# Kernel optimization log

Measured on AMD Instinct MI355X. Metric: run time of the kernel, lower is better.

The kernel has to match this reference:

```python
import jax, jax.numpy as jnp
import numpy as np

DIM = 768      # model dim
H = 12         # heads
HD = DIM // H  # head dim = 64
T = 8          # num_frames // 2 (video temporal frames)
SF = 8         # spec_frames (audio temporal frames)
AP = 196       # audio patches per frame
VP = 196       # video patches per frame
B = 4          # batch
SCALE = HD ** (-0.5)  # 0.125


def setup_inputs() -> dict:
    key = jax.random.key(0)
    ks = jax.random.split(key, 12)
    n = lambda k, shape, s=1.0: s * jax.random.normal(k, shape, dtype=jnp.float32)
    return {
        "s_x": n(ks[0], (2 + AP, B * SF, DIM)),
        "t_x": n(ks[1], (1 + VP, B * T, DIM)),
        "clip_space_pos": n(ks[2], (AP, DIM), SCALE),
        "vmae_space_pos": n(ks[3], (VP, DIM), SCALE),
        "clip_temporal_pos": n(ks[4], (SF, DIM), SCALE),
        "vmae_temporal_pos": n(ks[5], (T, DIM), SCALE),
        "q_w": n(ks[6], (DIM, DIM), 0.02),
        "q_b": jnp.zeros((DIM,), jnp.float32),
        "kv_w": n(ks[7], (2 * DIM, DIM), 0.02),
        "kv_b": jnp.zeros((2 * DIM,), jnp.float32),
        "proj_w": n(ks[8], (DIM, DIM), 0.02),
        "proj_b": jnp.zeros((DIM,), jnp.float32),
    }


def _prep(pat, space_pos, temp_pos, tt):
    # pat: (n, b*tt, d) ; rearrange 'n (b t) d -> b t n d', add space pos,
    # 'b t n d -> b n t d', add temporal pos, 'b n t d -> b (n t) d'
    n, bt, d = pat.shape
    b = bt // tt
    x = pat.reshape(n, b, tt, d).transpose(1, 2, 0, 3)      # b t n d
    x = x + space_pos                                        # (n,d) bcast
    x = x.transpose(0, 2, 1, 3) + temp_pos                   # b n t d + (t,d)
    return x.reshape(b, n * tt, d)


def reference(s_x, t_x, clip_space_pos, vmae_space_pos, clip_temporal_pos,
              vmae_temporal_pos, q_w, q_b, kv_w, kv_b, proj_w, proj_b):
    t_x_cls = t_x[:1]                                        # (1, b*T, d)
    s_pat = _prep(s_x[2:], clip_space_pos, clip_temporal_pos, SF)   # (b, AP*SF, d)
    t_pat = _prep(t_x[1:], vmae_space_pos, vmae_temporal_pos, T)    # (b, VP*T, d)

    b, N, d = t_pat.shape
    M = s_pat.shape[1]
    q = t_pat @ q_w.T + q_b                                  # (b, N, d)
    q = q.reshape(b, N, H, HD).transpose(0, 2, 1, 3)         # b h n hd
    kv = s_pat @ kv_w.T + kv_b                               # (b, M, 2d)
    kv = kv.reshape(b, M, 2, H, HD).transpose(2, 0, 3, 1, 4) # 2 b h m hd
    k, v = kv[0], kv[1]

    attn = jax.nn.softmax(jnp.einsum('bhnd,bhmd->bhnm', q * SCALE, k), axis=-1)
    out = jnp.einsum('bhnm,bhmd->bhnd', attn, v)             # b h n hd
    out = out.transpose(0, 2, 1, 3).reshape(b, N, d)         # b n d
    out = out @ proj_w.T + proj_b

    # 'b (n t) d -> n (b t) d'
    out = out.reshape(b, VP, T, d).transpose(1, 0, 2, 3).reshape(VP, b * T, d)
    return jnp.concatenate([t_x_cls, out], axis=0)           # (1+VP, b*T, d)
```

## Files before the change

kernel.cpp:

```cpp
#include <hip/hip_runtime.h>
#include <hip/hip_bf16.h>

#define DIM 768
#define NH 12
#define HD 64
#define NSEQ 1568
#define ROWS 6272
#define QSC2 0.18033688011112042f
#define AST 72

typedef __attribute__((ext_vector_type(8))) short short8;
typedef __attribute__((ext_vector_type(4))) float f32x4;
typedef __attribute__((ext_vector_type(4))) unsigned short u16x4;
typedef unsigned short ushort_t;
typedef unsigned int uint_t;

static __device__ __forceinline__ ushort_t f2bf(float f) {
    union { float f; uint_t u; } c; c.f = f;
    uint_t u = c.u + 0x7fffu + ((c.u >> 16) & 1u);
    return (ushort_t)(u >> 16);
}
static __device__ __forceinline__ int cvt_pk_bf16(float lo, float hi) {
    int r;
    asm("v_cvt_pk_bf16_f32 %0, %1, %2" : "=v"(r) : "v"(lo), "v"(hi));
    return r;
}
static __device__ __forceinline__ void glds16(const short* g, short* l) {
    __builtin_amdgcn_global_load_lds(
        (const __attribute__((address_space(1))) void*)g,
        (__attribute__((address_space(3))) void*)l, 16, 0, 0);
}

#define PREP_HALF (ROWS * (DIM / 8))
__global__ __launch_bounds__(256)
void prep2_bf(const float* __restrict__ src_t, const float* __restrict__ src_s,
              const float* __restrict__ vsp, const float* __restrict__ csp,
              const float* __restrict__ vtp, const float* __restrict__ ctp,
              short* __restrict__ dst_t, short* __restrict__ dst_s) {
    int idx = blockIdx.x * 256 + threadIdx.x;
    if (idx >= 2 * PREP_HALF) return;
    int sel = idx >= PREP_HALF;
    int i0  = sel ? idx - PREP_HALF : idx;
    const float* src  = sel ? src_s : src_t;
    const float* spos = sel ? csp : vsp;
    const float* tpos = sel ? ctp : vtp;
    short* dst = sel ? dst_s : dst_t;
    int d8  = i0 % (DIM / 8);
    int row = i0 / (DIM / 8);
    int b = row / NSEQ;
    int i = row % NSEQ;
    int n = i >> 3;
    int t = i & 7;
    const float4* s4 = reinterpret_cast<const float4*>(src + ((size_t)n * 32 + b * 8 + t) * DIM + d8 * 8);
    const float4* p4 = reinterpret_cast<const float4*>(spos + (size_t)n * DIM + d8 * 8);
    const float4* q4 = reinterpret_cast<const float4*>(tpos + (size_t)t * DIM + d8 * 8);
    union { int w[4]; short8 v; } o;
    float4 a0 = s4[0], a1 = s4[1], b0 = p4[0], b1 = p4[1], c0 = q4[0], c1 = q4[1];
    o.w[0] = cvt_pk_bf16(a0.x + b0.x + c0.x, a0.y + b0.y + c0.y);
    o.w[1] = cvt_pk_bf16(a0.z + b0.z + c0.z, a0.w + b0.w + c0.w);
    o.w[2] = cvt_pk_bf16(a1.x + b1.x + c1.x, a1.y + b1.y + c1.y);
    o.w[3] = cvt_pk_bf16(a1.z + b1.z + c1.z, a1.w + b1.w + c1.w);
    reinterpret_cast<short8*>(dst)[i0] = o.v;
}

#define W8 (DIM * DIM / 8)
__global__ __launch_bounds__(256)
void conv3_bf(const float* __restrict__ qw, const float* __restrict__ kvw,
              const float* __restrict__ pw, short* __restrict__ dq,
              short* __restrict__ dkv, short* __restrict__ dp) {
    int idx = blockIdx.x * 256 + threadIdx.x;
    if (idx >= 4 * W8) return;
    const float* src; short* dst; int off;
    if (idx < W8)            { src = qw;  dst = dq;  off = idx; }
    else if (idx < 3 * W8)   { src = kvw; dst = dkv; off = idx - W8; }
    else                     { src = pw;  dst = dp;  off = idx - 3 * W8; }
    const float4* s4 = reinterpret_cast<const float4*>(src + (size_t)off * 8);
    float4 a0 = s4[0], a1 = s4[1];
    union { int w[4]; short8 v; } o;
    o.w[0] = cvt_pk_bf16(a0.x, a0.y);
    o.w[1] = cvt_pk_bf16(a0.z, a0.w);
    o.w[2] = cvt_pk_bf16(a1.x, a1.y);
    o.w[3] = cvt_pk_bf16(a1.z, a1.w);
    reinterpret_cast<short8*>(dst)[off] = o.v;
}

__global__ __launch_bounds__(256)
void cls_kernel(const float* __restrict__ src, float* __restrict__ dst) {
    int idx = blockIdx.x * 256 + threadIdx.x;
    if (idx < 32 * DIM / 4)
        reinterpret_cast<float4*>(idx + (float4*)dst)[0] = reinterpret_cast<const float4*>(src)[idx];
}

__global__ __launch_bounds__(256)
void gemm_qkv(const short* __restrict__ tpat, const short* __restrict__ spat,
              const short* __restrict__ wq, const short* __restrict__ wkv,
              const float* __restrict__ q_b, const float* __restrict__ kv_b,
              ushort_t* __restrict__ qout, ushort_t* __restrict__ kout,
              ushort_t* __restrict__ vtout) {
    __shared__ short As[128 * 32];
    __shared__ short Ws[128 * 32];
    const int t = threadIdx.x;
    const int l = t & 63, w = t >> 6;
    const int li = l & 15, g = l >> 4;
    const int mode = (blockIdx.x >= 6);
    const short* A  = mode ? spat : tpat;
    const short* Wm = mode ? wkv : wq;
    const float* bias = mode ? kv_b : q_b;
    const int c0 = (mode ? (int)blockIdx.x - 6 : (int)blockIdx.x) * 128;
    const int r0 = blockIdx.y * 128;
    const int wrow = (w >> 1) * 64, wcol = (w & 1) * 64;

    f32x4 acc[4][4];
    #pragma unroll
    for (int i = 0; i < 4; ++i)
        #pragma unroll
        for (int j = 0; j < 4; ++j) acc[i][j] = (f32x4){0.f, 0.f, 0.f, 0.f};

    const short* Ag = A  + (size_t)(r0 + w * 32 + (l >> 2)) * DIM + (l & 3) * 8;
    const short* Wg = Wm + (size_t)(c0 + w * 32 + (l >> 2)) * DIM + (l & 3) * 8;
    short* Al0 = &As[(w * 32) * 32];
    short* Al1 = &As[(w * 32 + 16) * 32];
    short* Wl0 = &Ws[(w * 32) * 32];
    short* Wl1 = &Ws[(w * 32 + 16) * 32];

    for (int k0 = 0; k0 < DIM; k0 += 32) {
        glds16(Ag + k0,                       Al0);
        glds16(Ag + (size_t)16 * DIM + k0,    Al1);
        glds16(Wg + k0,                       Wl0);
        glds16(Wg + (size_t)16 * DIM + k0,    Wl1);
        __syncthreads();
        short8 af[4], wf[4];
        #pragma unroll
        for (int mi = 0; mi < 4; ++mi)
            af[mi] = *reinterpret_cast<const short8*>(&As[(wrow + mi * 16 + li) * 32 + g * 8]);
        #pragma unroll
        for (int ni = 0; ni < 4; ++ni)
            wf[ni] = *reinterpret_cast<const short8*>(&Ws[(wcol + ni * 16 + li) * 32 + g * 8]);
        __builtin_amdgcn_s_setprio(1);
        #pragma unroll
        for (int mi = 0; mi < 4; ++mi)
            #pragma unroll
            for (int ni = 0; ni < 4; ++ni)
                acc[mi][ni] = __builtin_amdgcn_mfma_f32_16x16x32_bf16(af[mi], wf[ni], acc[mi][ni], 0, 0, 0);
        __builtin_amdgcn_s_setprio(0);
        __syncthreads();
    }

    #pragma unroll
    for (int mi = 0; mi < 4; ++mi) {
        int rowbase = r0 + wrow + mi * 16 + g * 4;
        int b = rowbase / NSEQ;
        int ii = rowbase - b * NSEQ;
        #pragma unroll
        for (int ni = 0; ni < 4; ++ni) {
            int c = c0 + wcol + ni * 16 + li;
            float bv = bias[c];
            if (mode == 0) {
                int h = c >> 6, e = c & 63;
                size_t base = (((size_t)b * NH + h) * NSEQ + ii) * HD + e;
                #pragma unroll
                for (int rr = 0; rr < 4; ++rr)
                    qout[base + (size_t)rr * HD] = f2bf((acc[mi][ni][rr] + bv) * QSC2);
            } else {
                if (c < DIM) {
                    int h = c >> 6, e = c & 63;
                    size_t base = (((size_t)b * NH + h) * NSEQ + ii) * HD + e;
                    #pragma unroll
                    for (int rr = 0; rr < 4; ++rr)
                        kout[base + (size_t)rr * HD] = f2bf(acc[mi][ni][rr] + bv);
                } else {
                    int cc = c - DIM;
                    int h = cc >> 6, e = cc & 63;
                    union { int w2[2]; u16x4 v; } pk;
                    pk.w2[0] = cvt_pk_bf16(acc[mi][ni][0] + bv, acc[mi][ni][1] + bv);
                    pk.w2[1] = cvt_pk_bf16(acc[mi][ni][2] + bv, acc[mi][ni][3] + bv);
                    *reinterpret_cast<u16x4*>(vtout + (((size_t)b * NH + h) * HD + e) * NSEQ + ii) = pk.v;
                }
            }
        }
    }
}

__global__ __launch_bounds__(256)
void gemm_proj(const short* __restrict__ A, const short* __restrict__ Wm,
               const float* __restrict__ bias, float* __restrict__ out) {
    __shared__ short As[128 * 32];
    __shared__ short Ws[128 * 32];
    const int t = threadIdx.x;
    const int l = t & 63, w = t >> 6;
    const int li = l & 15, g = l >> 4;
    const int c0 = blockIdx.x * 128, r0 = blockIdx.y * 128;
    const int wrow = (w >> 1) * 64, wcol = (w & 1) * 64;

    f32x4 acc[4][4];
    #pragma unroll
    for (int i = 0; i < 4; ++i)
        #pragma unroll
        for (int j = 0; j < 4; ++j) acc[i][j] = (f32x4){0.f, 0.f, 0.f, 0.f};

    const short* Ag = A  + (size_t)(r0 + w * 32 + (l >> 2)) * DIM + (l & 3) * 8;
    const short* Wg = Wm + (size_t)(c0 + w * 32 + (l >> 2)) * DIM + (l & 3) * 8;
    short* Al0 = &As[(w * 32) * 32];
    short* Al1 = &As[(w * 32 + 16) * 32];
    short* Wl0 = &Ws[(w * 32) * 32];
    short* Wl1 = &Ws[(w * 32 + 16) * 32];

    for (int k0 = 0; k0 < DIM; k0 += 32) {
        glds16(Ag + k0,                       Al0);
        glds16(Ag + (size_t)16 * DIM + k0,    Al1);
        glds16(Wg + k0,                       Wl0);
        glds16(Wg + (size_t)16 * DIM + k0,    Wl1);
        __syncthreads();
        short8 af[4], wf[4];
        #pragma unroll
        for (int mi = 0; mi < 4; ++mi)
            af[mi] = *reinterpret_cast<const short8*>(&As[(wrow + mi * 16 + li) * 32 + g * 8]);
        #pragma unroll
        for (int ni = 0; ni < 4; ++ni)
            wf[ni] = *reinterpret_cast<const short8*>(&Ws[(wcol + ni * 16 + li) * 32 + g * 8]);
        __builtin_amdgcn_s_setprio(1);
        #pragma unroll
        for (int mi = 0; mi < 4; ++mi)
            #pragma unroll
            for (int ni = 0; ni < 4; ++ni)
                acc[mi][ni] = __builtin_amdgcn_mfma_f32_16x16x32_bf16(af[mi], wf[ni], acc[mi][ni], 0, 0, 0);
        __builtin_amdgcn_s_setprio(0);
        __syncthreads();
    }

    #pragma unroll
    for (int mi = 0; mi < 4; ++mi) {
        int rowbase = r0 + wrow + mi * 16 + g * 4;
        int b = rowbase / NSEQ;
        int ii = rowbase - b * NSEQ;
        #pragma unroll
        for (int ni = 0; ni < 4; ++ni) {
            int c = c0 + wcol + ni * 16 + li;
            float bv = bias[c];
            #pragma unroll
            for (int rr = 0; rr < 4; ++rr) {
                int i2 = ii + rr;
                int n = i2 >> 3, tt = i2 & 7;
                out[((size_t)(1 + n) * 32 + b * 8 + tt) * DIM + c] = acc[mi][ni][rr] + bv;
            }
        }
    }
}

__global__ __launch_bounds__(256)
void attn_bf(const short* __restrict__ q, const short* __restrict__ k,
             const short* __restrict__ vt, ushort_t* __restrict__ ao) {
    __shared__ short Qs[64 * AST];
    __shared__ short Ks[64 * AST];
    __shared__ short Vs[64 * AST];
    const int t = threadIdx.x, l = t & 63, w = t >> 6;
    const int li = l & 15, g = l >> 4;
    const int bh = blockIdx.y, b = bh / NH, h = bh % NH;
    const int q0 = blockIdx.x * 64;
    const short* qb = q + (size_t)bh * NSEQ * HD;
    const short* kb = k + (size_t)bh * NSEQ * HD;
    const short* vb = vt + (size_t)bh * HD * NSEQ;
    const int row = t >> 2, ch = t & 3;

    {
        int rs = (q0 + row < NSEQ) ? q0 + row : 0;
        const short* s = qb + (size_t)rs * HD + ch * 16;
        *reinterpret_cast<short8*>(&Qs[row * AST + ch * 16])     = *reinterpret_cast<const short8*>(s);
        *reinterpret_cast<short8*>(&Qs[row * AST + ch * 16 + 8]) = *reinterpret_cast<const short8*>(s + 8);
    }
    short8 kr0, kr1, vr0, vr1;
    {
        const short* s = kb + (size_t)row * HD + ch * 16;
        kr0 = *reinterpret_cast<const short8*>(s);
        kr1 = *reinterpret_cast<const short8*>(s + 8);
        const short* vs = vb + (size_t)row * NSEQ + ch * 16;
        vr0 = *reinterpret_cast<const short8*>(vs);
        vr1 = *reinterpret_cast<const short8*>(vs + 8);
    }
    __syncthreads();
    short8 qf[2];
    qf[0] = *reinterpret_cast<const short8*>(&Qs[(w * 16 + li) * AST + g * 8]);
    qf[1] = *reinterpret_cast<const short8*>(&Qs[(w * 16 + li) * AST + 32 + g * 8]);

    f32x4 oacc[4];
    #pragma unroll
    for (int i = 0; i < 4; ++i) oacc[i] = (f32x4){0.f, 0.f, 0.f, 0.f};
    float l_run = 0.f;
    const int addr0 = (li + ((2 * g) & 3) * 16) * 4;
    const int addr1 = (li + ((2 * g + 1) & 3) * 16) * 4;
    const int gh = g >> 1;

    for (int m0 = 0; m0 < NSEQ; m0 += 64) {
        *reinterpret_cast<short8*>(&Ks[row * AST + ch * 16])     = kr0;
        *reinterpret_cast<short8*>(&Ks[row * AST + ch * 16 + 8]) = kr1;
        *reinterpret_cast<short8*>(&Vs[row * AST + ch * 16])     = vr0;
        *reinterpret_cast<short8*>(&Vs[row * AST + ch * 16 + 8]) = vr1;
        __syncthreads();
        int m1 = m0 + 64;
        if (m1 < NSEQ) {
            int rs = (m1 + row < NSEQ) ? m1 + row : 0;
            const short* s = kb + (size_t)rs * HD + ch * 16;
            kr0 = *reinterpret_cast<const short8*>(s);
            kr1 = *reinterpret_cast<const short8*>(s + 8);
            int cs = (m1 + ch * 16 < NSEQ) ? ch : 0;
            const short* vs = vb + (size_t)row * NSEQ + m1 + cs * 16;
            vr0 = *reinterpret_cast<const short8*>(vs);
            vr1 = *reinterpret_cast<const short8*>(vs + 8);
        }

        f32x4 sacc[4];
        #pragma unroll
        for (int i = 0; i < 4; ++i) sacc[i] = (f32x4){0.f, 0.f, 0.f, 0.f};
        __builtin_amdgcn_s_setprio(1);
        #pragma unroll
        for (int jb = 0; jb < 4; ++jb) {
            short8 kf0 = *reinterpret_cast<const short8*>(&Ks[(jb * 16 + li) * AST + g * 8]);
            short8 kf1 = *reinterpret_cast<const short8*>(&Ks[(jb * 16 + li) * AST + 32 + g * 8]);
            sacc[jb] = __builtin_amdgcn_mfma_f32_16x16x32_bf16(kf0, qf[0], sacc[jb], 0, 0, 0);
            sacc[jb] = __builtin_amdgcn_mfma_f32_16x16x32_bf16(kf1, qf[1], sacc[jb], 0, 0, 0);
        }
        __builtin_amdgcn_s_setprio(0);
        if (m0 + 64 > NSEQ) {
            #pragma unroll
            for (int jb = 0; jb < 4; ++jb)
                #pragma unroll
                for (int r = 0; r < 4; ++r)
                    if (m0 + jb * 16 + g * 4 + r >= NSEQ) sacc[jb][r] = -1e30f;
        }

        float p[4][4];
        float ps[4];
        #pragma unroll
        for (int jb = 0; jb < 4; ++jb) {
            #pragma unroll
            for (int r = 0; r < 4; ++r)
                p[jb][r] = __builtin_amdgcn_exp2f(sacc[jb][r]);
            ps[jb] = (p[jb][0] + p[jb][1]) + (p[jb][2] + p[jb][3]);
        }
        float rowsum = (ps[0] + ps[1]) + (ps[2] + ps[3]);
        rowsum += __shfl_xor(rowsum, 16);
        rowsum += __shfl_xor(rowsum, 32);
        l_run += rowsum;

        int pw[4][2];
        #pragma unroll
        for (int jb = 0; jb < 4; ++jb) {
            pw[jb][0] = cvt_pk_bf16(p[jb][0], p[jb][1]);
            pw[jb][1] = cvt_pk_bf16(p[jb][2], p[jb][3]);
        }
        short8 pfrag[2];
        #pragma unroll
        for (int jb2 = 0; jb2 < 2; ++jb2) {
            int S0 = gh ? pw[jb2 * 2 + 1][0] : pw[jb2 * 2][0];
            int S1 = gh ? pw[jb2 * 2 + 1][1] : pw[jb2 * 2][1];
            union { int i[4]; short8 s; } fr;
            fr.i[0] = __builtin_amdgcn_ds_bpermute(addr0, S0);
            fr.i[1] = __builtin_amdgcn_ds_bpermute(addr0, S1);
            fr.i[2] = __builtin_amdgcn_ds_bpermute(addr1, S0);
            fr.i[3] = __builtin_amdgcn_ds_bpermute(addr1, S1);
            pfrag[jb2] = fr.s;
        }

        __builtin_amdgcn_s_setprio(1);
        #pragma unroll
        for (int nb = 0; nb < 4; ++nb)
            #pragma unroll
            for (int jb2 = 0; jb2 < 2; ++jb2) {
                short8 vf = *reinterpret_cast<const short8*>(&Vs[(nb * 16 + li) * AST + jb2 * 32 + g * 8]);
                oacc[nb] = __builtin_amdgcn_mfma_f32_16x16x32_bf16(vf, pfrag[jb2], oacc[nb], 0, 0, 0);
            }
        __builtin_amdgcn_s_setprio(0);
        __syncthreads();
    }

    int orow = q0 + w * 16 + li;
    if (orow < NSEQ) {
        float invl = 1.f / l_run;
        ushort_t* ob = ao + ((size_t)b * NSEQ + orow) * DIM + h * HD;
        #pragma unroll
        for (int nb = 0; nb < 4; ++nb) {
            union { int w2[2]; u16x4 v; } pk;
            pk.w2[0] = cvt_pk_bf16(oacc[nb][0] * invl, oacc[nb][1] * invl);
            pk.w2[1] = cvt_pk_bf16(oacc[nb][2] * invl, oacc[nb][3] * invl);
            *reinterpret_cast<u16x4*>(ob + nb * 16 + g * 4) = pk.v;
        }
    }
}

extern "C" void kernel_launch(void* const* d_in, const int* in_sizes, int n_in,
                              void* d_out, int out_size, void* d_ws, size_t ws_size,
                              hipStream_t stream) {
    const float* s_x    = (const float*)d_in[0];
    const float* t_x    = (const float*)d_in[1];
    const float* csp    = (const float*)d_in[2];
    const float* vsp    = (const float*)d_in[3];
    const float* ctp    = (const float*)d_in[4];
    const float* vtp    = (const float*)d_in[5];
    const float* q_w    = (const float*)d_in[6];
    const float* q_b    = (const float*)d_in[7];
    const float* kv_w   = (const float*)d_in[8];
    const float* kv_b   = (const float*)d_in[9];
    const float* proj_w = (const float*)d_in[10];
    const float* proj_b = (const float*)d_in[11];
    float* out = (float*)d_out;

    const size_t S2 = (size_t)ROWS * DIM;
    short* tpat = (short*)d_ws;
    short* spat = tpat + S2;
    short* qbf  = spat + S2;
    short* kbf  = qbf + S2;
    short* vtbf = kbf + S2;
    short* wq   = vtbf + S2;
    short* wkv  = wq + (size_t)DIM * DIM;
    short* wp   = wkv + (size_t)2 * DIM * DIM;

    prep2_bf<<<(2 * PREP_HALF + 255) / 256, 256, 0, stream>>>(
        t_x + (size_t)32 * DIM, s_x + (size_t)64 * DIM, vsp, csp, vtp, ctp, tpat, spat);
    conv3_bf<<<(4 * W8 + 255) / 256, 256, 0, stream>>>(q_w, kv_w, proj_w, wq, wkv, wp);
    cls_kernel<<<24, 256, 0, stream>>>(t_x, out);

    gemm_qkv<<<dim3(18, 49), 256, 0, stream>>>(tpat, spat, wq, wkv, q_b, kv_b,
                                               (ushort_t*)qbf, (ushort_t*)kbf, (ushort_t*)vtbf);
    attn_bf<<<dim3(25, 48), 256, 0, stream>>>(qbf, kbf, vtbf, (ushort_t*)tpat);
    gemm_proj<<<dim3(6, 49), 256, 0, stream>>>(tpat, wp, proj_b, out);
}
```

Baseline: 151.5 us.

## Double-buffer K/V in attention and process 32 query rows per warp

The attention kernel now handles 128 query rows per block (32 per warp as two 16-row halves), so each K/V tile staged in shared memory is reused across twice as many queries. K/V shared buffers are double-buffered, which leaves a single barrier per iteration and moves the next tile's LDS store ahead of the PV MFMAs. Q fragments are loaded straight from global memory into registers instead of passing through shared memory. The grid shrinks from 25 to 13 blocks in x, which halves the block count and raises per-thread register pressure, so occupancy may drop.

```diff
diff --git a/kernel.cpp b/kernel.cpp
--- a/kernel.cpp
+++ b/kernel.cpp
@@ -30,6 +30,41 @@
         (const __attribute__((address_space(1))) void*)g,
         (__attribute__((address_space(3))) void*)l, 16, 0, 0);
 }
+
+#define SM_HALF(S, PF, LR)                                                    \
+    {                                                                         \
+        float p_[4][4];                                                       \
+        _Pragma("unroll")                                                     \
+        for (int jb = 0; jb < 4; ++jb) {                                      \
+            _Pragma("unroll")                                                 \
+            for (int r = 0; r < 4; ++r)                                       \
+                p_[jb][r] = __builtin_amdgcn_exp2f(S[jb][r]);                 \
+        }                                                                     \
+        float rs_ = ((p_[0][0] + p_[0][1]) + (p_[0][2] + p_[0][3]))           \
+                  + ((p_[1][0] + p_[1][1]) + (p_[1][2] + p_[1][3]))           \
+                  + ((p_[2][0] + p_[2][1]) + (p_[2][2] + p_[2][3]))           \
+                  + ((p_[3][0] + p_[3][1]) + (p_[3][2] + p_[3][3]));          \
+        rs_ += __shfl_xor(rs_, 16);                                           \
+        rs_ += __shfl_xor(rs_, 32);                                           \
+        LR += rs_;                                                            \
+        int pw_[4][2];                                                        \
+        _Pragma("unroll")                                                     \
+        for (int jb = 0; jb < 4; ++jb) {                                      \
+            pw_[jb][0] = cvt_pk_bf16(p_[jb][0], p_[jb][1]);                   \
+            pw_[jb][1] = cvt_pk_bf16(p_[jb][2], p_[jb][3]);                   \
+        }                                                                     \
+        _Pragma("unroll")                                                     \
+        for (int jb2 = 0; jb2 < 2; ++jb2) {                                   \
+            int S0_ = gh ? pw_[jb2 * 2 + 1][0] : pw_[jb2 * 2][0];             \
+            int S1_ = gh ? pw_[jb2 * 2 + 1][1] : pw_[jb2 * 2][1];             \
+            union { int i[4]; short8 s; } fr_;                                \
+            fr_.i[0] = __builtin_amdgcn_ds_bpermute(addr0, S0_);              \
+            fr_.i[1] = __builtin_amdgcn_ds_bpermute(addr0, S1_);              \
+            fr_.i[2] = __builtin_amdgcn_ds_bpermute(addr1, S0_);              \
+            fr_.i[3] = __builtin_amdgcn_ds_bpermute(addr1, S1_);              \
+            PF[jb2] = fr_.s;                                                  \
+        }                                                                     \
+    }
 
 #define PREP_HALF (ROWS * (DIM / 8))
 __global__ __launch_bounds__(256)
@@ -88,7 +123,7 @@
 void cls_kernel(const float* __restrict__ src, float* __restrict__ dst) {
     int idx = blockIdx.x * 256 + threadIdx.x;
     if (idx < 32 * DIM / 4)
-        reinterpret_cast<float4*>(idx + (float4*)dst)[0] = reinterpret_cast<const float4*>(src)[idx];
+        reinterpret_cast<float4*>(dst)[idx] = reinterpret_cast<const float4*>(src)[idx];
 }
 
 __global__ __launch_bounds__(256)
@@ -250,24 +285,31 @@
 __global__ __launch_bounds__(256)
 void attn_bf(const short* __restrict__ q, const short* __restrict__ k,
              const short* __restrict__ vt, ushort_t* __restrict__ ao) {
-    __shared__ short Qs[64 * AST];
-    __shared__ short Ks[64 * AST];
-    __shared__ short Vs[64 * AST];
+    __shared__ short Ks[2 * 64 * AST];
+    __shared__ short Vs[2 * 64 * AST];
     const int t = threadIdx.x, l = t & 63, w = t >> 6;
     const int li = l & 15, g = l >> 4;
     const int bh = blockIdx.y, b = bh / NH, h = bh % NH;
-    const int q0 = blockIdx.x * 64;
+    const int q0 = blockIdx.x * 128;
     const short* qb = q + (size_t)bh * NSEQ * HD;
     const short* kb = k + (size_t)bh * NSEQ * HD;
     const short* vb = vt + (size_t)bh * HD * NSEQ;
     const int row = t >> 2, ch = t & 3;
 
+    short8 qf0[2], qf1[2];
     {
-        int rs = (q0 + row < NSEQ) ? q0 + row : 0;
-        const short* s = qb + (size_t)rs * HD + ch * 16;
-        *reinterpret_cast<short8*>(&Qs[row * AST + ch * 16])     = *reinterpret_cast<const short8*>(s);
-        *reinterpret_cast<short8*>(&Qs[row * AST + ch * 16 + 8]) = *reinterpret_cast<const short8*>(s + 8);
-    }
+        int r_ = q0 + w * 32 + li;
+        int rs = (r_ < NSEQ) ? r_ : 0;
+        const short* s = qb + (size_t)rs * HD + g * 8;
+        qf0[0] = *reinterpret_cast<const short8*>(s);
+        qf0[1] = *reinterpret_cast<const short8*>(s + 32);
+        r_ += 16;
+        rs = (r_ < NSEQ) ? r_ : 0;
+        s = qb + (size_t)rs * HD + g * 8;
+        qf1[0] = *reinterpret_cast<const short8*>(s);
+        qf1[1] = *reinterpret_cast<const short8*>(s + 32);
+    }
+
     short8 kr0, kr1, vr0, vr1;
     {
         const short* s = kb + (size_t)row * HD + ch * 16;
@@ -277,26 +319,30 @@
         vr0 = *reinterpret_cast<const short8*>(vs);
         vr1 = *reinterpret_cast<const short8*>(vs + 8);
     }
-    __syncthreads();
-    short8 qf[2];
-    qf[0] = *reinterpret_cast<const short8*>(&Qs[(w * 16 + li) * AST + g * 8]);
-    qf[1] = *reinterpret_cast<const short8*>(&Qs[(w * 16 + li) * AST + 32 + g * 8]);
-
-    f32x4 oacc[4];
+    *reinterpret_cast<short8*>(&Ks[row * AST + ch * 16])     = kr0;
+    *reinterpret_cast<short8*>(&Ks[row * AST + ch * 16 + 8]) = kr1;
+    *reinterpret_cast<short8*>(&Vs[row * AST + ch * 16])     = vr0;
+    *reinterpret_cast<short8*>(&Vs[row * AST + ch * 16 + 8]) = vr1;
+
+    f32x4 o0[4], o1[4];
     #pragma unroll
-    for (int i = 0; i < 4; ++i) oacc[i] = (f32x4){0.f, 0.f, 0.f, 0.f};
-    float l_run = 0.f;
+    for (int i = 0; i < 4; ++i) {
+        o0[i] = (f32x4){0.f, 0.f, 0.f, 0.f};
+        o1[i] = (f32x4){0.f, 0.f, 0.f, 0.f};
+    }
+    float lr0 = 0.f, lr1 = 0.f;
     const int addr0 = (li + ((2 * g) & 3) * 16) * 4;
     const int addr1 = (li + ((2 * g + 1) & 3) * 16) * 4;
     const int gh = g >> 1;
 
-    for (int m0 = 0; m0 < NSEQ; m0 += 64) {
-        *reinterpret_cast<short8*>(&Ks[row * AST + ch * 16])     = kr0;
-        *reinterpret_cast<short8*>(&Ks[row * AST + ch * 16 + 8]) = kr1;
-        *reinterpret_cast<short8*>(&Vs[row * AST + ch * 16])     = vr0;
-        *reinterpret_cast<short8*>(&Vs[row * AST + ch * 16 + 8]) = vr1;
+    int cur = 0;
+    for (int m0 = 0; m0 < NSEQ; m0 += 64, cur ^= 1) {
+        const short* Kc = &Ks[cur * 64 * AST];
+        const short* Vc = &Vs[cur * 64 * AST];
+        short* Kn = &Ks[(cur ^ 1) * 64 * AST];
+        short* Vn = &Vs[(cur ^ 1) * 64 * AST];
         __syncthreads();
-        int m1 = m0 + 64;
+        const int m1 = m0 + 64;
         if (m1 < NSEQ) {
             int rs = (m1 + row < NSEQ) ? m1 + row : 0;
             const short* s = kb + (size_t)rs * HD + ch * 16;
@@ -308,16 +354,21 @@
             vr1 = *reinterpret_cast<const short8*>(vs + 8);
         }
 
-        f32x4 sacc[4];
-        #pragma unroll
-        for (int i = 0; i < 4; ++i) sacc[i] = (f32x4){0.f, 0.f, 0.f, 0.f};
+        f32x4 s0[4], s1[4];
+        #pragma unroll
+        for (int i = 0; i < 4; ++i) {
+            s0[i] = (f32x4){0.f, 0.f, 0.f, 0.f};
+            s1[i] = (f32x4){0.f, 0.f, 0.f, 0.f};
+        }
         __builtin_amdgcn_s_setprio(1);
         #pragma unroll
         for (int jb = 0; jb < 4; ++jb) {
-            short8 kf0 = *reinterpret_cast<const short8*>(&Ks[(jb * 16 + li) * AST + g * 8]);
-            short8 kf1 = *reinterpret_cast<const short8*>(&Ks[(jb * 16 + li) * AST + 32 + g * 8]);
-            sacc[jb] = __builtin_amdgcn_mfma_f32_16x16x32_bf16(kf0, qf[0], sacc[jb], 0, 0, 0);
-            sacc[jb] = __builtin_amdgcn_mfma_f32_16x16x32_bf16(kf1, qf[1], sacc[jb], 0, 0, 0);
+            short8 kf0 = *reinterpret_cast<const short8*>(&Kc[(jb * 16 + li) * AST + g * 8]);
+            short8 kf1 = *reinterpret_cast<const short8*>(&Kc[(jb * 16 + li) * AST + 32 + g * 8]);
+            s0[jb] = __builtin_amdgcn_mfma_f32_16x16x32_bf16(kf0, qf0[0], s0[jb], 0, 0, 0);
+            s0[jb] = __builtin_amdgcn_mfma_f32_16x16x32_bf16(kf1, qf0[1], s0[jb], 0, 0, 0);
+            s1[jb] = __builtin_amdgcn_mfma_f32_16x16x32_bf16(kf0, qf1[0], s1[jb], 0, 0, 0);
+            s1[jb] = __builtin_amdgcn_mfma_f32_16x16x32_bf16(kf1, qf1[1], s1[jb], 0, 0, 0);
         }
         __builtin_amdgcn_s_setprio(0);
         if (m0 + 64 > NSEQ) {
@@ -325,40 +376,21 @@
             for (int jb = 0; jb < 4; ++jb)
                 #pragma unroll
                 for (int r = 0; r < 4; ++r)
-                    if (m0 + jb * 16 + g * 4 + r >= NSEQ) sacc[jb][r] = -1e30f;
-        }
-
-        float p[4][4];
-        float ps[4];
-        #pragma unroll
-        for (int jb = 0; jb < 4; ++jb) {
-            #pragma unroll
-            for (int r = 0; r < 4; ++r)
-                p[jb][r] = __builtin_amdgcn_exp2f(sacc[jb][r]);
-            ps[jb] = (p[jb][0] + p[jb][1]) + (p[jb][2] + p[jb][3]);
-        }
-        float rowsum = (ps[0] + ps[1]) + (ps[2] + ps[3]);
-        rowsum += __shfl_xor(rowsum, 16);
-        rowsum += __shfl_xor(rowsum, 32);
-        l_run += rowsum;
-
-        int pw[4][2];
-        #pragma unroll
-        for (int jb = 0; jb < 4; ++jb) {
-            pw[jb][0] = cvt_pk_bf16(p[jb][0], p[jb][1]);
-            pw[jb][1] = cvt_pk_bf16(p[jb][2], p[jb][3]);
-        }
-        short8 pfrag[2];
-        #pragma unroll
-        for (int jb2 = 0; jb2 < 2; ++jb2) {
-            int S0 = gh ? pw[jb2 * 2 + 1][0] : pw[jb2 * 2][0];
-            int S1 = gh ? pw[jb2 * 2 + 1][1] : pw[jb2 * 2][1];
-            union { int i[4]; short8 s; } fr;
-            fr.i[0] = __builtin_amdgcn_ds_bpermute(addr0, S0);
-            fr.i[1] = __builtin_amdgcn_ds_bpermute(addr0, S1);
-            fr.i[2] = __builtin_amdgcn_ds_bpermute(addr1, S0);
-            fr.i[3] = __builtin_amdgcn_ds_bpermute(addr1, S1);
-            pfrag[jb2] = fr.s;
+                    if (m0 + jb * 16 + g * 4 + r >= NSEQ) {
+                        s0[jb][r] = -1e30f;
+                        s1[jb][r] = -1e30f;
+                    }
+        }
+
+        short8 pf0[2], pf1[2];
+        SM_HALF(s0, pf0, lr0)
+        SM_HALF(s1, pf1, lr1)
+
+        if (m1 < NSEQ) {
+            *reinterpret_cast<short8*>(&Kn[row * AST + ch * 16])     = kr0;
+            *reinterpret_cast<short8*>(&Kn[row * AST + ch * 16 + 8]) = kr1;
+            *reinterpret_cast<short8*>(&Vn[row * AST + ch * 16])     = vr0;
+            *reinterpret_cast<short8*>(&Vn[row * AST + ch * 16 + 8]) = vr1;
         }
 
         __builtin_amdgcn_s_setprio(1);
@@ -366,23 +398,39 @@
         for (int nb = 0; nb < 4; ++nb)
             #pragma unroll
             for (int jb2 = 0; jb2 < 2; ++jb2) {
-                short8 vf = *reinterpret_cast<const short8*>(&Vs[(nb * 16 + li) * AST + jb2 * 32 + g * 8]);
-                oacc[nb] = __builtin_amdgcn_mfma_f32_16x16x32_bf16(vf, pfrag[jb2], oacc[nb], 0, 0, 0);
+                short8 vf = *reinterpret_cast<const short8*>(&Vc[(nb * 16 + li) * AST + jb2 * 32 + g * 8]);
+                o0[nb] = __builtin_amdgcn_mfma_f32_16x16x32_bf16(vf, pf0[jb2], o0[nb], 0, 0, 0);
+                o1[nb] = __builtin_amdgcn_mfma_f32_16x16x32_bf16(vf, pf1[jb2], o1[nb], 0, 0, 0);
             }
         __builtin_amdgcn_s_setprio(0);
-        __syncthreads();
-    }
-
-    int orow = q0 + w * 16 + li;
-    if (orow < NSEQ) {
-        float invl = 1.f / l_run;
-        ushort_t* ob = ao + ((size_t)b * NSEQ + orow) * DIM + h * HD;
-        #pragma unroll
-        for (int nb = 0; nb < 4; ++nb) {
-            union { int w2[2]; u16x4 v; } pk;
-            pk.w2[0] = cvt_pk_bf16(oacc[nb][0] * invl, oacc[nb][1] * invl);
-            pk.w2[1] = cvt_pk_bf16(oacc[nb][2] * invl, oacc[nb][3] * invl);
-            *reinterpret_cast<u16x4*>(ob + nb * 16 + g * 4) = pk.v;
+    }
+
+    {
+        int orow = q0 + w * 32 + li;
+        if (orow < NSEQ) {
+            float invl = 1.f / lr0;
+            ushort_t* ob = ao + ((size_t)b * NSEQ + orow) * DIM + h * HD;
+            #pragma unroll
+            for (int nb = 0; nb < 4; ++nb) {
+                union { int w2[2]; u16x4 v; } pk;
+                pk.w2[0] = cvt_pk_bf16(o0[nb][0] * invl, o0[nb][1] * invl);
+                pk.w2[1] = cvt_pk_bf16(o0[nb][2] * invl, o0[nb][3] * invl);
+                *reinterpret_cast<u16x4*>(ob + nb * 16 + g * 4) = pk.v;
+            }
+        }
+    }
+    {
+        int orow = q0 + w * 32 + 16 + li;
+        if (orow < NSEQ) {
+            float invl = 1.f / lr1;
+            ushort_t* ob = ao + ((size_t)b * NSEQ + orow) * DIM + h * HD;
+            #pragma unroll
+            for (int nb = 0; nb < 4; ++nb) {
+                union { int w2[2]; u16x4 v; } pk;
+                pk.w2[0] = cvt_pk_bf16(o1[nb][0] * invl, o1[nb][1] * invl);
+                pk.w2[1] = cvt_pk_bf16(o1[nb][2] * invl, o1[nb][3] * invl);
+                *reinterpret_cast<u16x4*>(ob + nb * 16 + g * 4) = pk.v;
+            }
         }
     }
 }
@@ -421,6 +469,6 @@
 
     gemm_qkv<<<dim3(18, 49), 256, 0, stream>>>(tpat, spat, wq, wkv, q_b, kv_b,
                                                (ushort_t*)qbf, (ushort_t*)kbf, (ushort_t*)vtbf);
-    attn_bf<<<dim3(25, 48), 256, 0, stream>>>(qbf, kbf, vtbf, (ushort_t*)tpat);
+    attn_bf<<<dim3(13, 48), 256, 0, stream>>>(qbf, kbf, vtbf, (ushort_t*)tpat);
     gemm_proj<<<dim3(6, 49), 256, 0, stream>>>(tpat, wp, proj_b, out);
 }
```

After: 152.0 us. About the same (+0.4%).
